# Kernel optimization log

Hardware: AMD Instinct MI355X
Metric: run time of the kernel (lower is better)

Reference implementation:

```python
import jax, jax.numpy as jnp
from jax import lax
import numpy as np

B, T, DD, DS, H = 512, 365, 5, 27, 256


def setup_inputs() -> dict:
    key = jax.random.key(0)
    ks = jax.random.split(key, 12)
    s = lambda fan_in: 1.0 / np.sqrt(fan_in)
    return {
        "x_dynamic": jax.random.normal(ks[0], (B, T, DD), jnp.float32),
        "x_static": jax.random.normal(ks[1], (B, DS), jnp.float32),
        "Wi": jax.random.normal(ks[2], (DS, H), jnp.float32) * s(DS),
        "bi": jax.random.normal(ks[3], (H,), jnp.float32) * s(DS),
        "Wf": jax.random.normal(ks[4], (DS, H), jnp.float32) * s(DS),
        "bf": jax.random.normal(ks[5], (H,), jnp.float32) * s(DS),
        "Wg": jax.random.normal(ks[6], (DD + H, H), jnp.float32) * s(DD + H),
        "bg": jax.random.normal(ks[7], (H,), jnp.float32) * s(DD + H),
        "Wo": jax.random.normal(ks[8], (DD + H, H), jnp.float32) * s(DD + H),
        "bo": jax.random.normal(ks[9], (H,), jnp.float32) * s(DD + H),
        "Wh": jax.random.normal(ks[10], (H, 1), jnp.float32) * s(H),
        "bh": jax.random.normal(ks[11], (1,), jnp.float32) * s(H),
    }


def reference(x_dynamic, x_static, Wi, bi, Wf, bf, Wg, bg, Wo, bo, Wh, bh):
    # Entity-aware gates depend only on static input -> compute once, reuse every step.
    i = jax.nn.sigmoid(x_static @ Wi + bi)  # [B, H]
    f = jax.nn.sigmoid(x_static @ Wf + bf)  # [B, H]

    bsz = x_dynamic.shape[0]
    hid = Wi.shape[1]
    h0 = jnp.zeros((bsz, hid), x_dynamic.dtype)
    c0 = jnp.zeros((bsz, hid), x_dynamic.dtype)

    def step(carry, x_t):
        h, c = carry
        comb = jnp.concatenate([x_t, h], axis=1)          # [B, DD+H]
        g = jnp.tanh(comb @ Wg + bg)
        o = jax.nn.sigmoid(comb @ Wo + bo)
        c_next = f * c + i * g
        h_next = o * jnp.tanh(c_next)
        return (h_next, c_next), None

    xs = jnp.swapaxes(x_dynamic, 0, 1)  # [T, B, DD]
    (h, _), _ = lax.scan(step, (h0, c0), xs)

    # Dropout is identity in eval mode.
    return h @ Wh + bh  # [B, 1]
```

## Files before the change

### kernel.cpp

```cpp
#include <hip/hip_runtime.h>

#define B_   512
#define T_   365
#define DD_  5
#define DS_  27
#define H_   256
#define ROWS 2
#define NBLK (B_ / ROWS)
#define NW   8
#define NTHR (NW * 64)

typedef _Float16 half8_t __attribute__((ext_vector_type(8)));
typedef float    f32x4   __attribute__((ext_vector_type(4)));

#define LOG2E_ 1.4426950408889634f

__device__ __forceinline__ float sigmoid_f(float x) {
    return __builtin_amdgcn_rcpf(1.0f + __builtin_amdgcn_exp2f(-x * LOG2E_));
}
__device__ __forceinline__ float tanh_f(float x) {
    return 1.0f - 2.0f * __builtin_amdgcn_rcpf(1.0f + __builtin_amdgcn_exp2f(2.0f * LOG2E_ * x));
}

__global__ __launch_bounds__(NTHR, 2)
void ealstm_kernel(const float* __restrict__ xdyn,
                   const float* __restrict__ xstat,
                   const float* __restrict__ Wi, const float* __restrict__ bi,
                   const float* __restrict__ Wf, const float* __restrict__ bf_,
                   const float* __restrict__ Wg, const float* __restrict__ bg,
                   const float* __restrict__ Wo, const float* __restrict__ bo,
                   const float* __restrict__ Wh, const float* __restrict__ bh,
                   float* __restrict__ out)
{
    const int tid = threadIdx.x;
    const int l   = tid & 63;
    const int w   = tid >> 6;
    const int blk = blockIdx.x;
    const int b0  = blk * ROWS;

    __shared__ __align__(16) _Float16 hbuf[2][16][264];
    __shared__ float xsh[ROWS][T_ * DD_];
    __shared__ float presh[2][H_][2];
    __shared__ float red[NW];

    {
        _Float16* hz = &hbuf[0][0][0];
        for (int i = tid; i < 2 * 16 * 264; i += NTHR) hz[i] = (_Float16)0.0f;
    }
    for (int i = tid; i < ROWS * T_ * DD_; i += NTHR) {
        int r   = i / (T_ * DD_);
        int rem = i - r * (T_ * DD_);
        xsh[r][rem] = xdyn[(size_t)(b0 + r) * (T_ * DD_) + rem];
    }

    const int colW = w * 32;
    const int lg   = l >> 4;
    const int lm   = l & 15;
    half8_t Bf[2][2][8];
    {
#pragma unroll
        for (int m = 0; m < 2; ++m) {
            const float* Ws = (m == 0) ? Wg : Wo;
#pragma unroll
            for (int tt = 0; tt < 2; ++tt) {
#pragma unroll
                for (int ks = 0; ks < 8; ++ks) {
                    int col = colW + tt * 16 + lm;
                    int k   = ks * 32 + 8 * lg;
                    const float* p = Ws + (size_t)(DD_ + k) * H_ + col;
                    half8_t v;
#pragma unroll
                    for (int i = 0; i < 8; ++i) v[i] = (_Float16)p[(size_t)i * H_];
                    Bf[m][tt][ks] = v;
                }
            }
        }
    }

    const int oc   = tid & 255;
    const int orow = tid >> 8;
    const int ob   = b0 + orow;

    float iG, fG;
    {
        float ai = bi[oc], af = bf_[oc];
        for (int d = 0; d < DS_; ++d) {
            float xv = xstat[ob * DS_ + d];
            ai += xv * Wi[d * H_ + oc];
            af += xv * Wf[d * H_ + oc];
        }
        iG = sigmoid_f(ai);
        fG = sigmoid_f(af);
    }
    float Wgx[DD_], Wox[DD_];
#pragma unroll
    for (int d = 0; d < DD_; ++d) {
        Wgx[d] = Wg[d * H_ + oc];
        Wox[d] = Wo[d * H_ + oc];
    }
    const float bgv = bg[oc], bov = bo[oc];

    float cst = 0.0f, hlast = 0.0f;

    half8_t Af[8];
    {
        half8_t z;
#pragma unroll
        for (int i = 0; i < 8; ++i) z[i] = (_Float16)0.0f;
#pragma unroll
        for (int ks = 0; ks < 8; ++ks) Af[ks] = z;
    }
    const bool areal = (lm < ROWS);

    __syncthreads();

    for (int t = 0; t < T_; ++t) {
        const int cur = t & 1;
        const int nxt = cur ^ 1;

        if (areal) {
#pragma unroll
            for (int ks = 0; ks < 8; ++ks)
                Af[ks] = *(const half8_t*)&hbuf[cur][lm][ks * 32 + 8 * lg];
        }

        f32x4 accG0 = {0.f,0.f,0.f,0.f}, accG1 = {0.f,0.f,0.f,0.f};
        f32x4 accO0 = {0.f,0.f,0.f,0.f}, accO1 = {0.f,0.f,0.f,0.f};
#pragma unroll
        for (int ks = 0; ks < 8; ++ks) {
            accG0 = __builtin_amdgcn_mfma_f32_16x16x32_f16(Af[ks], Bf[0][0][ks], accG0, 0, 0, 0);
            accG1 = __builtin_amdgcn_mfma_f32_16x16x32_f16(Af[ks], Bf[0][1][ks], accG1, 0, 0, 0);
            accO0 = __builtin_amdgcn_mfma_f32_16x16x32_f16(Af[ks], Bf[1][0][ks], accO0, 0, 0, 0);
            accO1 = __builtin_amdgcn_mfma_f32_16x16x32_f16(Af[ks], Bf[1][1][ks], accO1, 0, 0, 0);
        }

        if (l < 16) {
            int c0 = colW + lm;
            int c1 = colW + 16 + lm;
            *(float2*)&presh[0][c0][0] = make_float2(accG0[0], accG0[1]);
            *(float2*)&presh[0][c1][0] = make_float2(accG1[0], accG1[1]);
            *(float2*)&presh[1][c0][0] = make_float2(accO0[0], accO0[1]);
            *(float2*)&presh[1][c1][0] = make_float2(accO1[0], accO1[1]);
        }
        __syncthreads();

        {
            const float* xt = &xsh[orow][t * DD_];
            float xg = bgv, xo = bov;
#pragma unroll
            for (int d = 0; d < DD_; ++d) {
                float xv = xt[d];
                xg += xv * Wgx[d];
                xo += xv * Wox[d];
            }
            float pg = presh[0][oc][orow] + xg;
            float po = presh[1][oc][orow] + xo;
            float g  = tanh_f(pg);
            float o  = sigmoid_f(po);
            cst   = fG * cst + iG * g;
            hlast = o * tanh_f(cst);
            hbuf[nxt][orow][oc] = (_Float16)hlast;
        }
        __syncthreads();
    }

    float v = hlast * Wh[oc];
#pragma unroll
    for (int off = 32; off > 0; off >>= 1)
        v += __shfl_down(v, off);
    if (l == 0) red[w] = v;
    __syncthreads();
    if (tid < ROWS) {
        out[b0 + tid] = red[tid * 4 + 0] + red[tid * 4 + 1]
                      + red[tid * 4 + 2] + red[tid * 4 + 3] + bh[0];
    }
}

extern "C" void kernel_launch(void* const* d_in, const int* in_sizes, int n_in,
                              void* d_out, int out_size, void* d_ws, size_t ws_size,
                              hipStream_t stream) {
    (void)in_sizes; (void)n_in; (void)out_size; (void)d_ws; (void)ws_size;
    const float* xdyn  = (const float*)d_in[0];
    const float* xstat = (const float*)d_in[1];
    const float* Wi    = (const float*)d_in[2];
    const float* bi    = (const float*)d_in[3];
    const float* Wf    = (const float*)d_in[4];
    const float* bf    = (const float*)d_in[5];
    const float* Wg    = (const float*)d_in[6];
    const float* bg    = (const float*)d_in[7];
    const float* Wo    = (const float*)d_in[8];
    const float* bo    = (const float*)d_in[9];
    const float* Wh    = (const float*)d_in[10];
    const float* bh    = (const float*)d_in[11];
    float* out = (float*)d_out;

    hipLaunchKernelGGL(ealstm_kernel, dim3(NBLK), dim3(NTHR), 0, stream,
                       xdyn, xstat, Wi, bi, Wf, bf, Wg, bg, Wo, bo, Wh, bh, out);
}
```

Measured before the change: 322.8 us.

## Fuse gate epilogue into MFMA lanes and drop one barrier per step

The gate activations and cell update now run directly in the 16 lanes per wave that hold the MFMA accumulator rows, instead of staging pre-activations through shared memory and redistributing them across all 512 threads. This removes the presh buffer and one __syncthreads per timestep, and the input projection is computed before the MFMAs so it can overlap them. The cost is a serial epilogue of 4 elements in 16 lanes per wave rather than 1 element per thread. The final output now reads the fp16-rounded h from shared memory, which adds a small precision loss.

```diff
diff --git a/kernel.cpp b/kernel.cpp
--- a/kernel.cpp
+++ b/kernel.cpp
@@ -35,12 +35,10 @@
     const int tid = threadIdx.x;
     const int l   = tid & 63;
     const int w   = tid >> 6;
-    const int blk = blockIdx.x;
-    const int b0  = blk * ROWS;
+    const int b0  = blockIdx.x * ROWS;
 
     __shared__ __align__(16) _Float16 hbuf[2][16][264];
     __shared__ float xsh[ROWS][T_ * DD_];
-    __shared__ float presh[2][H_][2];
     __shared__ float red[NW];
 
     {
@@ -77,30 +75,37 @@
         }
     }
 
-    const int oc   = tid & 255;
-    const int orow = tid >> 8;
-    const int ob   = b0 + orow;
-
-    float iG, fG;
-    {
-        float ai = bi[oc], af = bf_[oc];
-        for (int d = 0; d < DS_; ++d) {
-            float xv = xstat[ob * DS_ + d];
-            ai += xv * Wi[d * H_ + oc];
-            af += xv * Wf[d * H_ + oc];
-        }
-        iG = sigmoid_f(ai);
-        fG = sigmoid_f(af);
-    }
-    float Wgx[DD_], Wox[DD_];
-#pragma unroll
-    for (int d = 0; d < DD_; ++d) {
-        Wgx[d] = Wg[d * H_ + oc];
-        Wox[d] = Wo[d * H_ + oc];
-    }
-    const float bgv = bg[oc], bov = bo[oc];
-
-    float cst = 0.0f, hlast = 0.0f;
+    const int c0 = colW + lm;
+    const int c1 = c0 + 16;
+    const bool epi = (l < 16);
+
+    float iG[2][2], fG[2][2], cst[2][2];
+    float Wgx[DD_][2], Wox[DD_][2], bgv[2], bov[2];
+    if (epi) {
+#pragma unroll
+        for (int ci = 0; ci < 2; ++ci) {
+            const int c = ci ? c1 : c0;
+            bgv[ci] = bg[c];
+            bov[ci] = bo[c];
+#pragma unroll
+            for (int d = 0; d < DD_; ++d) {
+                Wgx[d][ci] = Wg[d * H_ + c];
+                Wox[d][ci] = Wo[d * H_ + c];
+            }
+#pragma unroll
+            for (int r = 0; r < 2; ++r) {
+                float ai = bi[c], af = bf_[c];
+                for (int d = 0; d < DS_; ++d) {
+                    float xv = xstat[(b0 + r) * DS_ + d];
+                    ai += xv * Wi[d * H_ + c];
+                    af += xv * Wf[d * H_ + c];
+                }
+                iG[r][ci]  = sigmoid_f(ai);
+                fG[r][ci]  = sigmoid_f(af);
+                cst[r][ci] = 0.0f;
+            }
+        }
+    }
 
     half8_t Af[8];
     {
@@ -122,6 +127,24 @@
 #pragma unroll
             for (int ks = 0; ks < 8; ++ks)
                 Af[ks] = *(const half8_t*)&hbuf[cur][lm][ks * 32 + 8 * lg];
+        }
+
+        float xgv[2][2], xov[2][2];
+        if (epi) {
+#pragma unroll
+            for (int r = 0; r < 2; ++r) {
+                float g0 = bgv[0], g1 = bgv[1], o0 = bov[0], o1 = bov[1];
+#pragma unroll
+                for (int d = 0; d < DD_; ++d) {
+                    float xv = xsh[r][t * DD_ + d];
+                    g0 += xv * Wgx[d][0];
+                    g1 += xv * Wgx[d][1];
+                    o0 += xv * Wox[d][0];
+                    o1 += xv * Wox[d][1];
+                }
+                xgv[r][0] = g0; xgv[r][1] = g1;
+                xov[r][0] = o0; xov[r][1] = o1;
+            }
         }
 
         f32x4 accG0 = {0.f,0.f,0.f,0.f}, accG1 = {0.f,0.f,0.f,0.f};
@@ -134,37 +157,30 @@
             accO1 = __builtin_amdgcn_mfma_f32_16x16x32_f16(Af[ks], Bf[1][1][ks], accO1, 0, 0, 0);
         }
 
-        if (l < 16) {
-            int c0 = colW + lm;
-            int c1 = colW + 16 + lm;
-            *(float2*)&presh[0][c0][0] = make_float2(accG0[0], accG0[1]);
-            *(float2*)&presh[0][c1][0] = make_float2(accG1[0], accG1[1]);
-            *(float2*)&presh[1][c0][0] = make_float2(accO0[0], accO0[1]);
-            *(float2*)&presh[1][c1][0] = make_float2(accO1[0], accO1[1]);
+        if (epi) {
+#pragma unroll
+            for (int r = 0; r < 2; ++r) {
+                float pg0 = accG0[r] + xgv[r][0];
+                float pg1 = accG1[r] + xgv[r][1];
+                float po0 = accO0[r] + xov[r][0];
+                float po1 = accO1[r] + xov[r][1];
+                float g0 = tanh_f(pg0), g1 = tanh_f(pg1);
+                float o0 = sigmoid_f(po0), o1 = sigmoid_f(po1);
+                cst[r][0] = fG[r][0] * cst[r][0] + iG[r][0] * g0;
+                cst[r][1] = fG[r][1] * cst[r][1] + iG[r][1] * g1;
+                float h0 = o0 * tanh_f(cst[r][0]);
+                float h1 = o1 * tanh_f(cst[r][1]);
+                hbuf[nxt][r][c0] = (_Float16)h0;
+                hbuf[nxt][r][c1] = (_Float16)h1;
+            }
         }
         __syncthreads();
-
-        {
-            const float* xt = &xsh[orow][t * DD_];
-            float xg = bgv, xo = bov;
-#pragma unroll
-            for (int d = 0; d < DD_; ++d) {
-                float xv = xt[d];
-                xg += xv * Wgx[d];
-                xo += xv * Wox[d];
-            }
-            float pg = presh[0][oc][orow] + xg;
-            float po = presh[1][oc][orow] + xo;
-            float g  = tanh_f(pg);
-            float o  = sigmoid_f(po);
-            cst   = fG * cst + iG * g;
-            hlast = o * tanh_f(cst);
-            hbuf[nxt][orow][oc] = (_Float16)hlast;
-        }
-        __syncthreads();
-    }
-
-    float v = hlast * Wh[oc];
+    }
+
+    const int fin  = T_ & 1;
+    const int oc   = tid & 255;
+    const int orow = tid >> 8;
+    float v = (float)hbuf[fin][orow][oc] * Wh[oc];
 #pragma unroll
     for (int off = 32; off > 0; off >>= 1)
         v += __shfl_down(v, off);
```

Result: slower. 441.9 us (+36.9%).

## Redistribute MFMA gate outputs via wave shuffles, dropping shared staging and a barrier

Applied to the files above, without the earlier changes.

Each wave now owns exactly the 64 (row, column) outputs its MFMAs produce. Lanes fetch their pre-activations from the accumulator lanes with __shfl instead of staging them in a shared presh buffer. This removes one shared-memory round trip and one __syncthreads per timestep of the recurrence. The input projection is also computed before the MFMA chain so it can overlap. The final hidden state is read back from the fp16 hbuf instead of an fp32 register, which slightly lowers output precision.

```diff
diff --git a/kernel.cpp b/kernel.cpp
--- a/kernel.cpp
+++ b/kernel.cpp
@@ -35,12 +35,10 @@
     const int tid = threadIdx.x;
     const int l   = tid & 63;
     const int w   = tid >> 6;
-    const int blk = blockIdx.x;
-    const int b0  = blk * ROWS;
+    const int b0  = blockIdx.x * ROWS;
 
     __shared__ __align__(16) _Float16 hbuf[2][16][264];
     __shared__ float xsh[ROWS][T_ * DD_];
-    __shared__ float presh[2][H_][2];
     __shared__ float red[NW];
 
     {
@@ -77,30 +75,30 @@
         }
     }
 
-    const int oc   = tid & 255;
-    const int orow = tid >> 8;
-    const int ob   = b0 + orow;
+    const int r_l = (l >> 4) & 1;
+    const int ch  = l >> 5;
+    const int c_l = colW + ch * 16 + lm;
+    const int s_l = lm;
 
-    float iG, fG;
+    float Wgx[DD_], Wox[DD_];
+#pragma unroll
+    for (int d = 0; d < DD_; ++d) {
+        Wgx[d] = Wg[d * H_ + c_l];
+        Wox[d] = Wo[d * H_ + c_l];
+    }
+    const float bgv = bg[c_l], bov = bo[c_l];
+
+    float iG, fG, cst = 0.0f;
     {
-        float ai = bi[oc], af = bf_[oc];
+        float ai = bi[c_l], af = bf_[c_l];
         for (int d = 0; d < DS_; ++d) {
-            float xv = xstat[ob * DS_ + d];
-            ai += xv * Wi[d * H_ + oc];
-            af += xv * Wf[d * H_ + oc];
+            float xv = xstat[(b0 + r_l) * DS_ + d];
+            ai += xv * Wi[d * H_ + c_l];
+            af += xv * Wf[d * H_ + c_l];
         }
         iG = sigmoid_f(ai);
         fG = sigmoid_f(af);
     }
-    float Wgx[DD_], Wox[DD_];
-#pragma unroll
-    for (int d = 0; d < DD_; ++d) {
-        Wgx[d] = Wg[d * H_ + oc];
-        Wox[d] = Wo[d * H_ + oc];
-    }
-    const float bgv = bg[oc], bov = bo[oc];
-
-    float cst = 0.0f, hlast = 0.0f;
 
     half8_t Af[8];
     {
@@ -124,6 +122,14 @@
                 Af[ks] = *(const half8_t*)&hbuf[cur][lm][ks * 32 + 8 * lg];
         }
 
+        float xg = bgv, xo = bov;
+#pragma unroll
+        for (int d = 0; d < DD_; ++d) {
+            float xv = xsh[r_l][t * DD_ + d];
+            xg += xv * Wgx[d];
+            xo += xv * Wox[d];
+        }
+
         f32x4 accG0 = {0.f,0.f,0.f,0.f}, accG1 = {0.f,0.f,0.f,0.f};
         f32x4 accO0 = {0.f,0.f,0.f,0.f}, accO1 = {0.f,0.f,0.f,0.f};
 #pragma unroll
@@ -134,37 +140,28 @@
             accO1 = __builtin_amdgcn_mfma_f32_16x16x32_f16(Af[ks], Bf[1][1][ks], accO1, 0, 0, 0);
         }
 
-        if (l < 16) {
-            int c0 = colW + lm;
-            int c1 = colW + 16 + lm;
-            *(float2*)&presh[0][c0][0] = make_float2(accG0[0], accG0[1]);
-            *(float2*)&presh[0][c1][0] = make_float2(accG1[0], accG1[1]);
-            *(float2*)&presh[1][c0][0] = make_float2(accO0[0], accO0[1]);
-            *(float2*)&presh[1][c1][0] = make_float2(accO1[0], accO1[1]);
-        }
-        __syncthreads();
+        float g00 = __shfl(accG0[0], s_l), g01 = __shfl(accG0[1], s_l);
+        float g10 = __shfl(accG1[0], s_l), g11 = __shfl(accG1[1], s_l);
+        float o00 = __shfl(accO0[0], s_l), o01 = __shfl(accO0[1], s_l);
+        float o10 = __shfl(accO1[0], s_l), o11 = __shfl(accO1[1], s_l);
+        float pg = ch ? (r_l ? g11 : g10) : (r_l ? g01 : g00);
+        float po = ch ? (r_l ? o11 : o10) : (r_l ? o01 : o00);
+        pg += xg;
+        po += xo;
 
-        {
-            const float* xt = &xsh[orow][t * DD_];
-            float xg = bgv, xo = bov;
-#pragma unroll
-            for (int d = 0; d < DD_; ++d) {
-                float xv = xt[d];
-                xg += xv * Wgx[d];
-                xo += xv * Wox[d];
-            }
-            float pg = presh[0][oc][orow] + xg;
-            float po = presh[1][oc][orow] + xo;
-            float g  = tanh_f(pg);
-            float o  = sigmoid_f(po);
-            cst   = fG * cst + iG * g;
-            hlast = o * tanh_f(cst);
-            hbuf[nxt][orow][oc] = (_Float16)hlast;
-        }
+        float g = tanh_f(pg);
+        float o = sigmoid_f(po);
+        cst = fG * cst + iG * g;
+        float hv = o * tanh_f(cst);
+        hbuf[nxt][r_l][c_l] = (_Float16)hv;
+
         __syncthreads();
     }
 
-    float v = hlast * Wh[oc];
+    const int fin  = T_ & 1;
+    const int oc   = tid & 255;
+    const int orow = tid >> 8;
+    float v = (float)hbuf[fin][orow][oc] * Wh[oc];
 #pragma unroll
     for (int off = 32; off > 0; off >>= 1)
         v += __shfl_down(v, off);
```

Measured after the change: 310.2 us. 3.9% less time.
